# Optimization experiments

Measured on AMD Instinct MI355X. Metric: run time of the kernel, lower is better.

Reference implementation:

```python
import jax, jax.numpy as jnp
import numpy as np

D_MODEL = 1024
N_HEADS = 16
FACTOR = 2
KEY_DIM = D_MODEL // N_HEADS            # 64
HEAD_DIM = D_MODEL * FACTOR // N_HEADS  # 128
SCALING = KEY_DIM ** -0.5
BSZ, SEQ = 2, 2048


def _rel_pos(slen):
    # angle: 1/10000**linspace(0,1,key_dim//2), each value repeated twice
    half = jnp.asarray(1.0) / jnp.power(10000.0, jnp.linspace(0.0, 1.0, KEY_DIM // 2))
    angle = jnp.repeat(half, 2)                              # [key_dim]
    decay = jnp.log(1.0 - 2.0 ** (-5.0 - jnp.arange(N_HEADS, dtype=jnp.float32)))  # [h], negative
    idx = jnp.arange(slen, dtype=jnp.float32)
    sin = jnp.sin(idx[:, None] * angle[None, :])             # [s, key_dim]
    cos = jnp.cos(idx[:, None] * angle[None, :])
    diff = idx[:, None] - idx[None, :]                       # [s, s]
    tril = diff >= 0
    mask = jnp.where(tril[None], jnp.exp(diff[None] * decay[:, None, None]), 0.0)  # [h, s, s]
    mask = mask / jnp.sqrt(mask.sum(axis=-1, keepdims=True))
    return sin, cos, mask


def _rotate_every_two(x):
    x1 = x[..., ::2]
    x2 = x[..., 1::2]
    return jnp.stack((-x2, x1), axis=-1).reshape(x.shape)


def _theta_shift(x, sin, cos):
    return x * cos + _rotate_every_two(x) * sin


def setup_inputs() -> dict:
    key = jax.random.key(0)
    ks = jax.random.split(key, 11)
    s = 1.0 / np.sqrt(D_MODEL)
    s2 = 1.0 / np.sqrt(D_MODEL * FACTOR)
    return {
        "x": jax.random.normal(ks[0], (BSZ, SEQ, D_MODEL), jnp.float32),
        "q_w": jax.random.uniform(ks[1], (D_MODEL, D_MODEL), jnp.float32, -s, s),
        "q_b": jax.random.uniform(ks[2], (D_MODEL,), jnp.float32, -s, s),
        "k_w": jax.random.uniform(ks[3], (D_MODEL, D_MODEL), jnp.float32, -s, s),
        "k_b": jax.random.uniform(ks[4], (D_MODEL,), jnp.float32, -s, s),
        "v_w": jax.random.uniform(ks[5], (D_MODEL, D_MODEL * FACTOR), jnp.float32, -s, s),
        "v_b": jax.random.uniform(ks[6], (D_MODEL * FACTOR,), jnp.float32, -s, s),
        "g_w": jax.random.uniform(ks[7], (D_MODEL, D_MODEL * FACTOR), jnp.float32, -s, s),
        "g_b": jax.random.uniform(ks[8], (D_MODEL * FACTOR,), jnp.float32, -s, s),
        "o_w": jax.random.uniform(ks[9], (D_MODEL * FACTOR, D_MODEL), jnp.float32, -s2, s2),
        "o_b": jax.random.uniform(ks[10], (D_MODEL,), jnp.float32, -s2, s2),
    }


def _forward(x, q_w, q_b, k_w, k_b, v_w, v_b, g_w, g_b, o_w, o_b):
    bsz, slen, _ = x.shape
    sin, cos, mask = _rel_pos(slen)
    q = x @ q_w + q_b
    k = (x @ k_w + k_b) * SCALING
    v = x @ v_w + v_b
    g = x @ g_w + g_b
    # [b, h, s, key_dim]
    q = q.reshape(bsz, slen, N_HEADS, KEY_DIM).transpose(0, 2, 1, 3)
    k = k.reshape(bsz, slen, N_HEADS, KEY_DIM).transpose(0, 2, 1, 3)
    qr = _theta_shift(q, sin, cos)
    kr = _theta_shift(k, sin, cos)
    vr = v.reshape(bsz, slen, N_HEADS, HEAD_DIM).transpose(0, 2, 1, 3)  # [b,h,s,head_dim]
    qk = jnp.einsum('bhmd,bhnd->bhmn', qr, kr) * mask                  # decay-masked scores
    denom = jnp.clip(jnp.abs(jax.lax.stop_gradient(qk).sum(axis=-1, keepdims=True)), 1.0, None)
    qk = qk / denom
    out = jnp.einsum('bhmn,bhnd->bhmd', qk, vr).transpose(0, 2, 1, 3)  # [b,s,h,head_dim]
    # per-head LayerNorm over head_dim, no affine
    mu = out.mean(axis=-1, keepdims=True)
    var = out.var(axis=-1, keepdims=True)
    out = (out - mu) / jnp.sqrt(var + 1e-5)
    out = out.reshape(bsz, slen, N_HEADS * HEAD_DIM)
    out = jax.nn.silu(g) * out
    return out @ o_w + o_b


def reference(x, q_w, q_b, k_w, k_b, v_w, v_b, g_w, g_b, o_w, o_b):
    return _forward(x, q_w, q_b, k_w, k_b, v_w, v_b, g_w, g_b, o_w, o_b)
```

## Files before the change

### kernel.cpp

```cpp
#include <hip/hip_runtime.h>
#include <hip/hip_bf16.h>


typedef __hip_bfloat16 bf16;
typedef short bf16x4 __attribute__((ext_vector_type(4)));
typedef short bf16x8 __attribute__((ext_vector_type(8)));
typedef float floatx4 __attribute__((ext_vector_type(4)));

#define B_SZ 2
#define SEQ 2048
#define NH 16
#define KD 64
#define HD 128

#define ASYNC16(gp, lp)                                                             \
  __builtin_amdgcn_global_load_lds(                                                 \
      (const __attribute__((address_space(1))) unsigned int*)(unsigned long long)(const void*)(gp), \
      (__attribute__((address_space(3))) unsigned int*)(unsigned int)(unsigned long long)(void*)(lp), \
      16, 0, 0)

__device__ __forceinline__ float b2f(bf16 x) { return __bfloat162float(x); }
__device__ __forceinline__ bf16 f2b(float x) { return __float2bfloat16(x); }

__global__ void convert_k(const float* __restrict__ in, bf16* __restrict__ out) {
  int i = blockIdx.x * 256 + threadIdx.x;
  float4 v = reinterpret_cast<const float4*>(in)[i];
  union { bf16 h[4]; bf16x4 v4; } u;
  u.h[0] = f2b(v.x); u.h[1] = f2b(v.y); u.h[2] = f2b(v.z); u.h[3] = f2b(v.w);
  reinterpret_cast<bf16x4*>(out)[i] = u.v4;
}

__global__ void transpose_k(const float* __restrict__ in, bf16* __restrict__ out,
                            int K, int N) {
  __shared__ float tile[32][33];
  int tx = threadIdx.x, ty = threadIdx.y;
  int n0 = blockIdx.x * 32, k0 = blockIdx.y * 32;
#pragma unroll
  for (int j = 0; j < 4; ++j)
    tile[ty + j * 8][tx] = in[(size_t)(k0 + ty + j * 8) * N + n0 + tx];
  __syncthreads();
#pragma unroll
  for (int j = 0; j < 4; ++j)
    out[(size_t)(n0 + ty + j * 8) * K + k0 + tx] = f2b(tile[tx][ty + j * 8]);
}

__global__ void vtrans_k(const bf16* __restrict__ in, bf16* __restrict__ out) {
  __shared__ bf16 tile[32][34];
  int tx = threadIdx.x, ty = threadIdx.y;
  int s0 = blockIdx.x * 32, c0 = blockIdx.y * 32;
  const bf16* src = in + (size_t)blockIdx.z * 2048 * 2048;
  bf16* dst = out + (size_t)blockIdx.z * 2048 * 2048;
#pragma unroll
  for (int j = 0; j < 4; ++j)
    tile[ty + j * 8][tx] = src[(size_t)(s0 + ty + j * 8) * 2048 + c0 + tx];
  __syncthreads();
#pragma unroll
  for (int j = 0; j < 4; ++j)
    dst[(size_t)(c0 + ty + j * 8) * 2048 + s0 + tx] = tile[tx][ty + j * 8];
}

template <int BM, int BN, int KDIM, int MODE>
__global__ __launch_bounds__(256, 2) void gemm_bt(
    const bf16* __restrict__ A, const bf16* __restrict__ Bt, int Ndim,
    const float* __restrict__ bias_q, const float* __restrict__ bias_k,
    const float* __restrict__ bias_v, const float* __restrict__ bias_g,
    float* __restrict__ outCqk, bf16* __restrict__ out_v,
    float* __restrict__ out_g, float* __restrict__ outF) {
  __shared__ bf16 As[BM * 32];
  __shared__ bf16 Bs[BN * 32];
  const int tid = threadIdx.x;
  const int wave = tid >> 6, lane = tid & 63;
  const int quad = lane >> 4, l16 = lane & 15;
  const int m0 = blockIdx.y * BM, n0 = blockIdx.x * BN;
  constexpr int FI = BM / 32;
  constexpr int FJ = BN / 32;
  const int wm = (wave >> 1) * (BM / 2), wn = (wave & 1) * (BN / 2);

  floatx4 acc[FI][FJ] = {};

  for (int k0 = 0; k0 < KDIM; k0 += 32) {
#pragma unroll
    for (int j = 0; j < BM / 64; ++j) {
      int cbase = (j * 4 + wave) * 64;
      int c = cbase + lane;
      const bf16* g = A + (size_t)(m0 + (c >> 2)) * KDIM + k0 + (c & 3) * 8;
      ASYNC16(g, &As[cbase * 8]);
    }
#pragma unroll
    for (int j = 0; j < BN / 64; ++j) {
      int cbase = (j * 4 + wave) * 64;
      int c = cbase + lane;
      const bf16* g = Bt + (size_t)(n0 + (c >> 2)) * KDIM + k0 + (c & 3) * 8;
      ASYNC16(g, &Bs[cbase * 8]);
    }
    __syncthreads();

    bf16x8 af[FI], bfr[FJ];
#pragma unroll
    for (int i = 0; i < FI; ++i)
      af[i] = *(const bf16x8*)&As[(wm + i * 16 + l16) * 32 + quad * 8];
#pragma unroll
    for (int j = 0; j < FJ; ++j)
      bfr[j] = *(const bf16x8*)&Bs[(wn + j * 16 + l16) * 32 + quad * 8];
#pragma unroll
    for (int i = 0; i < FI; ++i)
#pragma unroll
      for (int j = 0; j < FJ; ++j)
        acc[i][j] = __builtin_amdgcn_mfma_f32_16x16x32_bf16(af[i], bfr[j],
                                                            acc[i][j], 0, 0, 0);
    __syncthreads();
  }

#pragma unroll
  for (int i = 0; i < FI; ++i) {
#pragma unroll
    for (int j = 0; j < FJ; ++j) {
#pragma unroll
      for (int r = 0; r < 4; ++r) {
        int gm = m0 + wm + i * 16 + quad * 4 + r;
        int gn = n0 + wn + j * 16 + l16;
        float v = acc[i][j][r];
        if (MODE == 1) {
          v += bias_q[gn];
          outF[(size_t)gm * Ndim + gn] = v;
        } else {
          if (gn < 2048) {
            bool is_k = gn >= 1024;
            int jj = is_k ? gn - 1024 : gn;
            v += is_k ? bias_k[jj] : bias_q[jj];
            if (is_k) v *= 0.125f;
            outCqk[(size_t)gm * 2048 + gn] = v;
          } else if (gn < 4096) {
            int jj = gn - 2048;
            v += bias_v[jj];
            out_v[(size_t)gm * 2048 + jj] = f2b(v);
          } else {
            int jj = gn - 4096;
            v += bias_g[jj];
            out_g[(size_t)gm * 2048 + jj] = v;
          }
        }
      }
    }
  }
}

__global__ void router_k(const float* __restrict__ Cqk,
                         bf16* __restrict__ qh, bf16* __restrict__ ql,
                         bf16* __restrict__ kh, bf16* __restrict__ kl) {
  int t = blockIdx.x * 256 + threadIdx.x;
  int row = t >> 10, pc = t & 1023;
  int b = row >> 11, s = row & 2047;
  bool is_k = pc >= 512;
  int jj = (pc - (is_k ? 512 : 0)) * 2;
  int h = jj >> 6, d = jj & 63, ii = d >> 1;
  float2 v = *(const float2*)&Cqk[(size_t)row * 2048 + pc * 2];
  float half = exp2f(-(float)ii * (13.287712379549449f / 31.0f));
  float ang = (float)s * half;
  float sn = sinf(ang), cs = cosf(ang);
  float e = v.x * cs - v.y * sn;
  float o = v.y * cs + v.x * sn;
  bf16 eh = f2b(e), oh = f2b(o);
  bf16 el = f2b(e - b2f(eh)), ol = f2b(o - b2f(oh));
  size_t idx = (((size_t)b * NH + h) * SEQ + s) * KD + d;
  bf16* ph = is_k ? kh : qh;
  bf16* pl = is_k ? kl : ql;
  union { bf16 h2[2]; unsigned u; } uh, ul;
  uh.h2[0] = eh; uh.h2[1] = oh;
  ul.h2[0] = el; ul.h2[1] = ol;
  *(unsigned*)&ph[idx] = uh.u;
  *(unsigned*)&pl[idx] = ul.u;
}

__global__ __launch_bounds__(256, 4) void retention_k(
    const bf16* __restrict__ qh, const bf16* __restrict__ ql,
    const bf16* __restrict__ kh, const bf16* __restrict__ kl,
    const bf16* __restrict__ vT, const float* __restrict__ g,
    bf16* __restrict__ gated) {
  __shared__ bf16 KHs[2][32 * 64];
  __shared__ bf16 KLs[2][32 * 64];
  __shared__ bf16 Vs[2][128 * 32];
  __shared__ bf16 Pl[4][16 * 32];
  const int tid = threadIdx.x;
  const int wave = tid >> 6, lane = tid & 63;
  const int quad = lane >> 4, l16 = lane & 15;
  const int h = blockIdx.y, b = blockIdx.z;
  const int bh = b * NH + h;
  const int bt = 31 - blockIdx.x;
  const int m0 = bt * 64 + wave * 16;
  const int ntiles = 2 * bt + 2;

  const float t = exp2f(-(float)(5 + h));
  const float lng = log1pf(-t);
  const float log2g = lng * 1.44269504088896340736f;

  float rf[4];
#pragma unroll
  for (int r = 0; r < 4; ++r) {
    int m = m0 + quad * 4 + r;
    float num = -expm1f((float)(m + 1) * lng);
    rf[r] = exp2f((float)m * log2g) * rsqrtf(num / t);
  }
  const float gstep = exp2f(-32.0f * log2g);
  const float cf0 = exp2f(-(float)l16 * log2g);
  const float cf1 = cf0 * exp2f(-16.0f * log2g);

  const size_t qoff = ((size_t)bh * SEQ + m0 + l16) * KD;
  bf16x8 aq0h = *(const bf16x8*)&qh[qoff + quad * 8];
  bf16x8 aq1h = *(const bf16x8*)&qh[qoff + 32 + quad * 8];
  bf16x8 aq0l = *(const bf16x8*)&ql[qoff + quad * 8];
  bf16x8 aq1l = *(const bf16x8*)&ql[qoff + 32 + quad * 8];

  floatx4 oacc[8] = {};
  float rowsum[4] = {0.f, 0.f, 0.f, 0.f};

  const bf16* khb = kh + (size_t)bh * SEQ * KD;
  const bf16* klb = kl + (size_t)bh * SEQ * KD;
  const bf16* vbase = vT + (size_t)bh * HD * SEQ;

  auto stage = [&](int nt, int buf) {
    const int n0s = nt * 32;
#pragma unroll
    for (int j = 0; j < 4; ++j) {
      int cc = wave * 4 + j;
      if (cc < 8) {
        const bf16* src = (cc < 4) ? khb : klb;
        bf16* dst = (cc < 4) ? KHs[buf] : KLs[buf];
        int r = ((cc & 3) * 8) + (lane >> 3);
        int s = lane & 7;
        int q = (s - r) & 7;
        ASYNC16(src + (size_t)(n0s + r) * KD + q * 8, &dst[(cc & 3) * 512]);
      } else {
        int r = (cc - 8) * 16 + (lane >> 2);
        int s = lane & 3;
        int q = (s - (r >> 1)) & 3;
        ASYNC16(vbase + (size_t)r * SEQ + n0s + q * 8, &Vs[buf][(cc - 8) * 512]);
      }
    }
  };

  stage(0, 0);
  for (int nt = 0; nt < ntiles; ++nt) {
    const int n0 = nt * 32;
    const int cur = nt & 1;
    asm volatile("s_waitcnt vmcnt(0) lgkmcnt(0)" ::: "memory");
    __syncthreads();
    {
      int pf = (nt + 1 < ntiles) ? nt + 1 : nt;
      stage(pf, cur ^ 1);
    }

    const bool active = (n0 <= m0 + 15);
    if (active) {
      floatx4 sc[2];
#pragma unroll
      for (int hh = 0; hh < 2; ++hh) {
        int krow = hh * 16 + l16;
        int c0 = ((quad + krow) & 7) * 8;
        int c1 = ((quad + 4 + krow) & 7) * 8;
        bf16x8 bkh0 = *(const bf16x8*)&KHs[cur][krow * 64 + c0];
        bf16x8 bkh1 = *(const bf16x8*)&KHs[cur][krow * 64 + c1];
        bf16x8 bkl0 = *(const bf16x8*)&KLs[cur][krow * 64 + c0];
        bf16x8 bkl1 = *(const bf16x8*)&KLs[cur][krow * 64 + c1];
        floatx4 z1 = {0.f, 0.f, 0.f, 0.f}, z2 = z1, z3 = z1;
        z1 = __builtin_amdgcn_mfma_f32_16x16x32_bf16(aq0h, bkh0, z1, 0, 0, 0);
        z2 = __builtin_amdgcn_mfma_f32_16x16x32_bf16(aq0l, bkh0, z2, 0, 0, 0);
        z3 = __builtin_amdgcn_mfma_f32_16x16x32_bf16(aq0h, bkl0, z3, 0, 0, 0);
        z1 = __builtin_amdgcn_mfma_f32_16x16x32_bf16(aq1h, bkh1, z1, 0, 0, 0);
        z2 = __builtin_amdgcn_mfma_f32_16x16x32_bf16(aq1l, bkh1, z2, 0, 0, 0);
        z3 = __builtin_amdgcn_mfma_f32_16x16x32_bf16(aq1h, bkl1, z3, 0, 0, 0);
        sc[hh] = z1 + z2 + z3;
      }

#pragma unroll
      for (int hh = 0; hh < 2; ++hh) {
        float cf = hh ? cf1 : cf0;
#pragma unroll
        for (int r = 0; r < 4; ++r) {
          int m = m0 + quad * 4 + r;
          int n = n0 + hh * 16 + l16;
          float p = (m >= n) ? sc[hh][r] * rf[r] * cf : 0.f;
          rowsum[r] += p;
          Pl[wave][(quad * 4 + r) * 32 + hh * 16 + l16] = f2b(p);
        }
      }
#pragma unroll
      for (int r = 0; r < 4; ++r) rf[r] *= gstep;

      asm volatile("s_waitcnt lgkmcnt(0)" ::: "memory");
      bf16x8 pa = *(const bf16x8*)&Pl[wave][l16 * 32 + quad * 8];

#pragma unroll
      for (int dt = 0; dt < 8; ++dt) {
        int vrow = dt * 16 + l16;
        bf16x8 bv = *(const bf16x8*)&Vs[cur][vrow * 32 + ((quad + (vrow >> 1)) & 3) * 8];
        oacc[dt] = __builtin_amdgcn_mfma_f32_16x16x32_bf16(pa, bv, oacc[dt], 0, 0, 0);
      }
    }
  }

  float inv_den[4];
#pragma unroll
  for (int r = 0; r < 4; ++r) {
    float v = rowsum[r];
    v += __shfl_xor(v, 1);
    v += __shfl_xor(v, 2);
    v += __shfl_xor(v, 4);
    v += __shfl_xor(v, 8);
    inv_den[r] = 1.0f / fmaxf(fabsf(v), 1.0f);
  }
  float s1[4] = {}, s2[4] = {};
#pragma unroll
  for (int dt = 0; dt < 8; ++dt) {
#pragma unroll
    for (int r = 0; r < 4; ++r) {
      float v = oacc[dt][r] * inv_den[r];
      oacc[dt][r] = v;
      s1[r] += v;
      s2[r] += v * v;
    }
  }
  float mean[4], istd[4];
#pragma unroll
  for (int r = 0; r < 4; ++r) {
    float a = s1[r], q2 = s2[r];
    a += __shfl_xor(a, 1); a += __shfl_xor(a, 2);
    a += __shfl_xor(a, 4); a += __shfl_xor(a, 8);
    q2 += __shfl_xor(q2, 1); q2 += __shfl_xor(q2, 2);
    q2 += __shfl_xor(q2, 4); q2 += __shfl_xor(q2, 8);
    mean[r] = a * (1.0f / 128.0f);
    float var = q2 * (1.0f / 128.0f) - mean[r] * mean[r];
    istd[r] = rsqrtf(fmaxf(var, 0.0f) + 1e-5f);
  }
#pragma unroll
  for (int dt = 0; dt < 8; ++dt) {
#pragma unroll
    for (int r = 0; r < 4; ++r) {
      int m = m0 + quad * 4 + r;
      int col = h * HD + dt * 16 + l16;
      float v = (oacc[dt][r] - mean[r]) * istd[r];
      float gv = g[((size_t)b * SEQ + m) * 2048 + col];
      float sg = gv / (1.0f + expf(-gv));
      gated[((size_t)b * SEQ + m) * 2048 + col] = f2b(sg * v);
    }
  }
}

extern "C" void kernel_launch(void* const* d_in, const int* in_sizes, int n_in,
                              void* d_out, int out_size, void* d_ws,
                              size_t ws_size, hipStream_t stream) {
  const float* x   = (const float*)d_in[0];
  const float* q_w = (const float*)d_in[1];
  const float* q_b = (const float*)d_in[2];
  const float* k_w = (const float*)d_in[3];
  const float* k_b = (const float*)d_in[4];
  const float* v_w = (const float*)d_in[5];
  const float* v_b = (const float*)d_in[6];
  const float* g_w = (const float*)d_in[7];
  const float* g_b = (const float*)d_in[8];
  const float* o_w = (const float*)d_in[9];
  const float* o_b = (const float*)d_in[10];

  char* ws = (char*)d_ws;
  bf16* Wt    = (bf16*)ws; ws += (size_t)6144 * 1024 * 2;
  bf16* oT    = (bf16*)ws; ws += (size_t)1024 * 2048 * 2;
  bf16* xb    = (bf16*)ws; ws += (size_t)4096 * 1024 * 2;
  float* Cqk  = (float*)ws; ws += (size_t)4096 * 2048 * 4;
  bf16* qhb   = (bf16*)ws; ws += (size_t)32 * 2048 * 64 * 2;
  bf16* qlb   = (bf16*)ws; ws += (size_t)32 * 2048 * 64 * 2;
  bf16* khb   = (bf16*)ws; ws += (size_t)32 * 2048 * 64 * 2;
  bf16* klb   = (bf16*)ws; ws += (size_t)32 * 2048 * 64 * 2;
  bf16* vTb   = (bf16*)ws; ws += (size_t)32 * 128 * 2048 * 2;
  float* gbuf = (float*)ws; ws += (size_t)2 * 2048 * 2048 * 4;
  bf16* gated = (bf16*)ws; ws += (size_t)4096 * 2048 * 2;
  bf16* vbuf  = gated;

  convert_k<<<(4096 * 1024 / 4) / 256, 256, 0, stream>>>(x, xb);

  dim3 tb(32, 8);
  transpose_k<<<dim3(1024 / 32, 1024 / 32), tb, 0, stream>>>(q_w, Wt, 1024, 1024);
  transpose_k<<<dim3(1024 / 32, 1024 / 32), tb, 0, stream>>>(k_w, Wt + (size_t)1024 * 1024, 1024, 1024);
  transpose_k<<<dim3(2048 / 32, 1024 / 32), tb, 0, stream>>>(v_w, Wt + (size_t)2048 * 1024, 1024, 2048);
  transpose_k<<<dim3(2048 / 32, 1024 / 32), tb, 0, stream>>>(g_w, Wt + (size_t)4096 * 1024, 1024, 2048);
  transpose_k<<<dim3(1024 / 32, 2048 / 32), tb, 0, stream>>>(o_w, oT, 2048, 1024);

  gemm_bt<128, 128, 1024, 0><<<dim3(6144 / 128, 4096 / 128), 256, 0, stream>>>(
      xb, Wt, 6144, q_b, k_b, v_b, g_b, Cqk, vbuf, gbuf, nullptr);

  vtrans_k<<<dim3(64, 64, B_SZ), tb, 0, stream>>>(vbuf, vTb);

  router_k<<<(4096 * 1024) / 256, 256, 0, stream>>>(Cqk, qhb, qlb, khb, klb);

  retention_k<<<dim3(32, NH, B_SZ), 256, 0, stream>>>(
      qhb, qlb, khb, klb, vTb, gbuf, gated);

  gemm_bt<128, 64, 2048, 1><<<dim3(1024 / 64, 4096 / 128), 256, 0, stream>>>(
      gated, oT, 1024, o_b, nullptr, nullptr, nullptr, nullptr, nullptr,
      nullptr, (float*)d_out);
}
```

Measured before the change: 372.2 us.

## Pair high and low causal query tiles per retention block to balance work

Each retention block now handles two 64-row query tiles, a late one and its mirrored early one, so every block does the same total causal work. The two tiles share the staged K and V tiles in shared memory, which halves the K/V loads for the low tile, and the grid shrinks from 32 to 16 blocks per head. In exchange, register pressure roughly doubles (two accumulator sets), so the launch bound drops from 4 to 2 waves per SIMD, and there are half as many blocks to hide latency.

```diff
diff --git a/kernel.cpp b/kernel.cpp
--- a/kernel.cpp
+++ b/kernel.cpp
@@ -172,7 +172,7 @@
   *(unsigned*)&pl[idx] = ul.u;
 }
 
-__global__ __launch_bounds__(256, 4) void retention_k(
+__global__ __launch_bounds__(256, 2) void retention_k(
     const bf16* __restrict__ qh, const bf16* __restrict__ ql,
     const bf16* __restrict__ kh, const bf16* __restrict__ kl,
     const bf16* __restrict__ vT, const float* __restrict__ g,
@@ -180,39 +180,51 @@
   __shared__ bf16 KHs[2][32 * 64];
   __shared__ bf16 KLs[2][32 * 64];
   __shared__ bf16 Vs[2][128 * 32];
-  __shared__ bf16 Pl[4][16 * 32];
+  __shared__ bf16 Plh[4][16 * 32];
+  __shared__ bf16 Pll[4][16 * 32];
   const int tid = threadIdx.x;
   const int wave = tid >> 6, lane = tid & 63;
   const int quad = lane >> 4, l16 = lane & 15;
   const int h = blockIdx.y, b = blockIdx.z;
   const int bh = b * NH + h;
-  const int bt = 31 - blockIdx.x;
-  const int m0 = bt * 64 + wave * 16;
-  const int ntiles = 2 * bt + 2;
+  const int bt_h = 31 - (int)blockIdx.x;
+  const int bt_l = (int)blockIdx.x;
+  const int m0h = bt_h * 64 + wave * 16;
+  const int m0l = bt_l * 64 + wave * 16;
+  const int ntiles = 2 * bt_h + 2;
+  const int lt_ntiles = 2 * bt_l + 2;
 
   const float t = exp2f(-(float)(5 + h));
   const float lng = log1pf(-t);
   const float log2g = lng * 1.44269504088896340736f;
 
-  float rf[4];
+  float rfh[4], rfl[4];
 #pragma unroll
   for (int r = 0; r < 4; ++r) {
-    int m = m0 + quad * 4 + r;
-    float num = -expm1f((float)(m + 1) * lng);
-    rf[r] = exp2f((float)m * log2g) * rsqrtf(num / t);
+    int mh = m0h + quad * 4 + r;
+    int ml = m0l + quad * 4 + r;
+    rfh[r] = exp2f((float)mh * log2g) *
+             rsqrtf(-expm1f((float)(mh + 1) * lng) / t);
+    rfl[r] = exp2f((float)ml * log2g) *
+             rsqrtf(-expm1f((float)(ml + 1) * lng) / t);
   }
   const float gstep = exp2f(-32.0f * log2g);
   const float cf0 = exp2f(-(float)l16 * log2g);
   const float cf1 = cf0 * exp2f(-16.0f * log2g);
 
-  const size_t qoff = ((size_t)bh * SEQ + m0 + l16) * KD;
-  bf16x8 aq0h = *(const bf16x8*)&qh[qoff + quad * 8];
-  bf16x8 aq1h = *(const bf16x8*)&qh[qoff + 32 + quad * 8];
-  bf16x8 aq0l = *(const bf16x8*)&ql[qoff + quad * 8];
-  bf16x8 aq1l = *(const bf16x8*)&ql[qoff + 32 + quad * 8];
-
-  floatx4 oacc[8] = {};
-  float rowsum[4] = {0.f, 0.f, 0.f, 0.f};
+  const size_t qoffh = ((size_t)bh * SEQ + m0h + l16) * KD;
+  const size_t qoffl = ((size_t)bh * SEQ + m0l + l16) * KD;
+  bf16x8 aq0h_h = *(const bf16x8*)&qh[qoffh + quad * 8];
+  bf16x8 aq1h_h = *(const bf16x8*)&qh[qoffh + 32 + quad * 8];
+  bf16x8 aq0l_h = *(const bf16x8*)&ql[qoffh + quad * 8];
+  bf16x8 aq1l_h = *(const bf16x8*)&ql[qoffh + 32 + quad * 8];
+  bf16x8 aq0h_l = *(const bf16x8*)&qh[qoffl + quad * 8];
+  bf16x8 aq1h_l = *(const bf16x8*)&qh[qoffl + 32 + quad * 8];
+  bf16x8 aq0l_l = *(const bf16x8*)&ql[qoffl + quad * 8];
+  bf16x8 aq1l_l = *(const bf16x8*)&ql[qoffl + 32 + quad * 8];
+
+  floatx4 oacch[8] = {}, oaccl[8] = {};
+  float rsh[4] = {0.f, 0.f, 0.f, 0.f}, rsl[4] = {0.f, 0.f, 0.f, 0.f};
 
   const bf16* khb = kh + (size_t)bh * SEQ * KD;
   const bf16* klb = kl + (size_t)bh * SEQ * KD;
@@ -250,100 +262,132 @@
       stage(pf, cur ^ 1);
     }
 
-    const bool active = (n0 <= m0 + 15);
-    if (active) {
-      floatx4 sc[2];
-#pragma unroll
-      for (int hh = 0; hh < 2; ++hh) {
-        int krow = hh * 16 + l16;
-        int c0 = ((quad + krow) & 7) * 8;
-        int c1 = ((quad + 4 + krow) & 7) * 8;
-        bf16x8 bkh0 = *(const bf16x8*)&KHs[cur][krow * 64 + c0];
-        bf16x8 bkh1 = *(const bf16x8*)&KHs[cur][krow * 64 + c1];
-        bf16x8 bkl0 = *(const bf16x8*)&KLs[cur][krow * 64 + c0];
-        bf16x8 bkl1 = *(const bf16x8*)&KLs[cur][krow * 64 + c1];
+    const bool hact = (n0 <= m0h + 15);
+    const bool lact = (n0 <= m0l + 15);
+
+    floatx4 sch[2], scl[2];
+#pragma unroll
+    for (int hh = 0; hh < 2; ++hh) {
+      int krow = hh * 16 + l16;
+      int c0 = ((quad + krow) & 7) * 8;
+      int c1 = ((quad + 4 + krow) & 7) * 8;
+      bf16x8 bkh0 = *(const bf16x8*)&KHs[cur][krow * 64 + c0];
+      bf16x8 bkh1 = *(const bf16x8*)&KHs[cur][krow * 64 + c1];
+      bf16x8 bkl0 = *(const bf16x8*)&KLs[cur][krow * 64 + c0];
+      bf16x8 bkl1 = *(const bf16x8*)&KLs[cur][krow * 64 + c1];
+      if (hact) {
         floatx4 z1 = {0.f, 0.f, 0.f, 0.f}, z2 = z1, z3 = z1;
-        z1 = __builtin_amdgcn_mfma_f32_16x16x32_bf16(aq0h, bkh0, z1, 0, 0, 0);
-        z2 = __builtin_amdgcn_mfma_f32_16x16x32_bf16(aq0l, bkh0, z2, 0, 0, 0);
-        z3 = __builtin_amdgcn_mfma_f32_16x16x32_bf16(aq0h, bkl0, z3, 0, 0, 0);
-        z1 = __builtin_amdgcn_mfma_f32_16x16x32_bf16(aq1h, bkh1, z1, 0, 0, 0);
-        z2 = __builtin_amdgcn_mfma_f32_16x16x32_bf16(aq1l, bkh1, z2, 0, 0, 0);
-        z3 = __builtin_amdgcn_mfma_f32_16x16x32_bf16(aq1h, bkl1, z3, 0, 0, 0);
-        sc[hh] = z1 + z2 + z3;
-      }
-
-#pragma unroll
-      for (int hh = 0; hh < 2; ++hh) {
-        float cf = hh ? cf1 : cf0;
-#pragma unroll
-        for (int r = 0; r < 4; ++r) {
-          int m = m0 + quad * 4 + r;
-          int n = n0 + hh * 16 + l16;
-          float p = (m >= n) ? sc[hh][r] * rf[r] * cf : 0.f;
-          rowsum[r] += p;
-          Pl[wave][(quad * 4 + r) * 32 + hh * 16 + l16] = f2b(p);
+        z1 = __builtin_amdgcn_mfma_f32_16x16x32_bf16(aq0h_h, bkh0, z1, 0, 0, 0);
+        z2 = __builtin_amdgcn_mfma_f32_16x16x32_bf16(aq0l_h, bkh0, z2, 0, 0, 0);
+        z3 = __builtin_amdgcn_mfma_f32_16x16x32_bf16(aq0h_h, bkl0, z3, 0, 0, 0);
+        z1 = __builtin_amdgcn_mfma_f32_16x16x32_bf16(aq1h_h, bkh1, z1, 0, 0, 0);
+        z2 = __builtin_amdgcn_mfma_f32_16x16x32_bf16(aq1l_h, bkh1, z2, 0, 0, 0);
+        z3 = __builtin_amdgcn_mfma_f32_16x16x32_bf16(aq1h_h, bkl1, z3, 0, 0, 0);
+        sch[hh] = z1 + z2 + z3;
+      }
+      if (lact) {
+        floatx4 z1 = {0.f, 0.f, 0.f, 0.f}, z2 = z1, z3 = z1;
+        z1 = __builtin_amdgcn_mfma_f32_16x16x32_bf16(aq0h_l, bkh0, z1, 0, 0, 0);
+        z2 = __builtin_amdgcn_mfma_f32_16x16x32_bf16(aq0l_l, bkh0, z2, 0, 0, 0);
+        z3 = __builtin_amdgcn_mfma_f32_16x16x32_bf16(aq0h_l, bkl0, z3, 0, 0, 0);
+        z1 = __builtin_amdgcn_mfma_f32_16x16x32_bf16(aq1h_l, bkh1, z1, 0, 0, 0);
+        z2 = __builtin_amdgcn_mfma_f32_16x16x32_bf16(aq1l_l, bkh1, z2, 0, 0, 0);
+        z3 = __builtin_amdgcn_mfma_f32_16x16x32_bf16(aq1h_l, bkl1, z3, 0, 0, 0);
+        scl[hh] = z1 + z2 + z3;
+      }
+    }
+
+#pragma unroll
+    for (int hh = 0; hh < 2; ++hh) {
+      float cf = hh ? cf1 : cf0;
+#pragma unroll
+      for (int r = 0; r < 4; ++r) {
+        int n = n0 + hh * 16 + l16;
+        if (hact) {
+          int m = m0h + quad * 4 + r;
+          float p = (m >= n) ? sch[hh][r] * rfh[r] * cf : 0.f;
+          rsh[r] += p;
+          Plh[wave][(quad * 4 + r) * 32 + hh * 16 + l16] = f2b(p);
         }
-      }
-#pragma unroll
-      for (int r = 0; r < 4; ++r) rf[r] *= gstep;
-
-      asm volatile("s_waitcnt lgkmcnt(0)" ::: "memory");
-      bf16x8 pa = *(const bf16x8*)&Pl[wave][l16 * 32 + quad * 8];
-
-#pragma unroll
-      for (int dt = 0; dt < 8; ++dt) {
-        int vrow = dt * 16 + l16;
-        bf16x8 bv = *(const bf16x8*)&Vs[cur][vrow * 32 + ((quad + (vrow >> 1)) & 3) * 8];
-        oacc[dt] = __builtin_amdgcn_mfma_f32_16x16x32_bf16(pa, bv, oacc[dt], 0, 0, 0);
-      }
+        if (lact) {
+          int m = m0l + quad * 4 + r;
+          float p = (m >= n) ? scl[hh][r] * rfl[r] * cf : 0.f;
+          rsl[r] += p;
+          Pll[wave][(quad * 4 + r) * 32 + hh * 16 + l16] = f2b(p);
+        }
+      }
+    }
+#pragma unroll
+    for (int r = 0; r < 4; ++r) {
+      rfh[r] *= gstep;
+      if (nt + 1 < lt_ntiles) rfl[r] *= gstep;
+    }
+
+    asm volatile("s_waitcnt lgkmcnt(0)" ::: "memory");
+    bf16x8 pah, pal;
+    if (hact) pah = *(const bf16x8*)&Plh[wave][l16 * 32 + quad * 8];
+    if (lact) pal = *(const bf16x8*)&Pll[wave][l16 * 32 + quad * 8];
+
+#pragma unroll
+    for (int dt = 0; dt < 8; ++dt) {
+      int vrow = dt * 16 + l16;
+      bf16x8 bv = *(const bf16x8*)&Vs[cur][vrow * 32 + ((quad + (vrow >> 1)) & 3) * 8];
+      if (hact)
+        oacch[dt] = __builtin_amdgcn_mfma_f32_16x16x32_bf16(pah, bv, oacch[dt], 0, 0, 0);
+      if (lact)
+        oaccl[dt] = __builtin_amdgcn_mfma_f32_16x16x32_bf16(pal, bv, oaccl[dt], 0, 0, 0);
     }
   }
 
-  float inv_den[4];
-#pragma unroll
-  for (int r = 0; r < 4; ++r) {
-    float v = rowsum[r];
-    v += __shfl_xor(v, 1);
-    v += __shfl_xor(v, 2);
-    v += __shfl_xor(v, 4);
-    v += __shfl_xor(v, 8);
-    inv_den[r] = 1.0f / fmaxf(fabsf(v), 1.0f);
-  }
-  float s1[4] = {}, s2[4] = {};
-#pragma unroll
-  for (int dt = 0; dt < 8; ++dt) {
+  auto finalize = [&](floatx4* oacc, float* rowsum, int m0) {
+    float inv_den[4];
 #pragma unroll
     for (int r = 0; r < 4; ++r) {
-      float v = oacc[dt][r] * inv_den[r];
-      oacc[dt][r] = v;
-      s1[r] += v;
-      s2[r] += v * v;
-    }
-  }
-  float mean[4], istd[4];
-#pragma unroll
-  for (int r = 0; r < 4; ++r) {
-    float a = s1[r], q2 = s2[r];
-    a += __shfl_xor(a, 1); a += __shfl_xor(a, 2);
-    a += __shfl_xor(a, 4); a += __shfl_xor(a, 8);
-    q2 += __shfl_xor(q2, 1); q2 += __shfl_xor(q2, 2);
-    q2 += __shfl_xor(q2, 4); q2 += __shfl_xor(q2, 8);
-    mean[r] = a * (1.0f / 128.0f);
-    float var = q2 * (1.0f / 128.0f) - mean[r] * mean[r];
-    istd[r] = rsqrtf(fmaxf(var, 0.0f) + 1e-5f);
-  }
-#pragma unroll
-  for (int dt = 0; dt < 8; ++dt) {
+      float v = rowsum[r];
+      v += __shfl_xor(v, 1);
+      v += __shfl_xor(v, 2);
+      v += __shfl_xor(v, 4);
+      v += __shfl_xor(v, 8);
+      inv_den[r] = 1.0f / fmaxf(fabsf(v), 1.0f);
+    }
+    float s1[4] = {}, s2[4] = {};
+#pragma unroll
+    for (int dt = 0; dt < 8; ++dt) {
+#pragma unroll
+      for (int r = 0; r < 4; ++r) {
+        float v = oacc[dt][r] * inv_den[r];
+        oacc[dt][r] = v;
+        s1[r] += v;
+        s2[r] += v * v;
+      }
+    }
+    float mean[4], istd[4];
 #pragma unroll
     for (int r = 0; r < 4; ++r) {
-      int m = m0 + quad * 4 + r;
-      int col = h * HD + dt * 16 + l16;
-      float v = (oacc[dt][r] - mean[r]) * istd[r];
-      float gv = g[((size_t)b * SEQ + m) * 2048 + col];
-      float sg = gv / (1.0f + expf(-gv));
-      gated[((size_t)b * SEQ + m) * 2048 + col] = f2b(sg * v);
-    }
-  }
+      float a = s1[r], q2 = s2[r];
+      a += __shfl_xor(a, 1); a += __shfl_xor(a, 2);
+      a += __shfl_xor(a, 4); a += __shfl_xor(a, 8);
+      q2 += __shfl_xor(q2, 1); q2 += __shfl_xor(q2, 2);
+      q2 += __shfl_xor(q2, 4); q2 += __shfl_xor(q2, 8);
+      mean[r] = a * (1.0f / 128.0f);
+      float var = q2 * (1.0f / 128.0f) - mean[r] * mean[r];
+      istd[r] = rsqrtf(fmaxf(var, 0.0f) + 1e-5f);
+    }
+#pragma unroll
+    for (int dt = 0; dt < 8; ++dt) {
+#pragma unroll
+      for (int r = 0; r < 4; ++r) {
+        int m = m0 + quad * 4 + r;
+        int col = h * HD + dt * 16 + l16;
+        float v = (oacc[dt][r] - mean[r]) * istd[r];
+        float gv = g[((size_t)b * SEQ + m) * 2048 + col];
+        float sg = gv / (1.0f + expf(-gv));
+        gated[((size_t)b * SEQ + m) * 2048 + col] = f2b(sg * v);
+      }
+    }
+  };
+  finalize(oacch, rsh, m0h);
+  finalize(oaccl, rsl, m0l);
 }
 
 extern "C" void kernel_launch(void* const* d_in, const int* in_sizes, int n_in,
@@ -391,7 +435,7 @@
 
   router_k<<<(4096 * 1024) / 256, 256, 0, stream>>>(Cqk, qhb, qlb, khb, klb);
 
-  retention_k<<<dim3(32, NH, B_SZ), 256, 0, stream>>>(
+  retention_k<<<dim3(16, NH, B_SZ), 256, 0, stream>>>(
       qhb, qlb, khb, klb, vTb, gbuf, gated);
 
   gemm_bt<128, 64, 2048, 1><<<dim3(1024 / 64, 4096 / 128), 256, 0, stream>>>(
```

After: 356.4 us. -4.2%, faster.
